# Kernel tuning notes

Hardware: AMD Instinct MI355X
Metric: run time of the kernel (lower is better)

## Reference

```python
import jax, jax.numpy as jnp
import numpy as np

H, C = 3, 64          # heads, out_channels
NEG_SLOPE = 0.2       # PyG GATConv leaky_relu default
LN_EPS = 1e-5


def setup_inputs() -> dict:
    key = jax.random.key(0)
    ks = jax.random.split(key, 20)
    N, E, D_in, edge_dim = 50000, 800000, 64, 5
    g = lambda k, shape: (jax.random.normal(k, shape, dtype=jnp.float32) * 0.1)
    return {
        "x": jax.random.normal(ks[0], (N, D_in), dtype=jnp.float32),
        "edge_attr": jax.random.normal(ks[1], (E, edge_dim), dtype=jnp.float32),
        "lin_w": g(ks[2], (D_in, H * C)),          # GATConv.lin (bias=False)
        "att_src": g(ks[3], (H, C)),
        "att_dst": g(ks[4], (H, C)),
        "lin_edge_w": g(ks[5], (edge_dim, H * C)),  # GATConv.lin_edge (bias=False)
        "att_edge": g(ks[6], (H, C)),
        "gat_bias": jnp.zeros((H * C,), jnp.float32),
        "w1": g(ks[7], (H * C, C)),
        "b1": jnp.zeros((C,), jnp.float32),
        "ln1_g": jnp.ones((C,), jnp.float32),
        "ln1_b": jnp.zeros((C,), jnp.float32),
        "w2": g(ks[8], (C, C)),
        "b2": jnp.zeros((C,), jnp.float32),
        "ln2_g": jnp.ones((C,), jnp.float32),
        "ln2_b": jnp.zeros((C,), jnp.float32),
        "edge_index": jax.random.randint(ks[9], (2, E), 0, N),
    }


def layer_norm(x, g, b):
    m = jnp.mean(x, axis=-1, keepdims=True)
    v = jnp.mean((x - m) ** 2, axis=-1, keepdims=True)
    return (x - m) * jax.lax.rsqrt(v + LN_EPS) * g + b


def gat_conv(x, edge_index, edge_attr, lin_w, att_src, att_dst,
             lin_edge_w, att_edge, gat_bias):
    N = x.shape[0]
    src, dst = edge_index[0], edge_index[1]

    # add_self_loops=True with fill_value='mean': self-loop edge_attr is the
    # per-node mean of incoming edge attributes (0 if node has no in-edges).
    attr_sum = jax.ops.segment_sum(edge_attr, dst, num_segments=N)       # [N, edge_dim]
    cnt = jax.ops.segment_sum(jnp.ones((dst.shape[0],), edge_attr.dtype), dst, num_segments=N)
    loop_attr = attr_sum / jnp.maximum(cnt, 1.0)[:, None]
    loop = jnp.arange(N, dtype=src.dtype)
    src = jnp.concatenate([src, loop])
    dst = jnp.concatenate([dst, loop])
    ea = jnp.concatenate([edge_attr, loop_attr], axis=0)                  # [E2, edge_dim]

    xs = (x @ lin_w).reshape(N, H, C)                                     # [N, H, C]
    a_src = jnp.einsum('nhc,hc->nh', xs, att_src)                         # [N, H]
    a_dst = jnp.einsum('nhc,hc->nh', xs, att_dst)                         # [N, H]
    e = (ea @ lin_edge_w).reshape(-1, H, C)                               # [E2, H, C]
    a_edge = jnp.einsum('ehc,hc->eh', e, att_edge)                        # [E2, H]

    logits = a_src[src] + a_dst[dst] + a_edge                             # [E2, H]
    logits = jnp.where(logits >= 0, logits, NEG_SLOPE * logits)           # leaky_relu

    # segment softmax over incoming edges of each dst node (self loops ensure non-empty)
    lmax = jax.ops.segment_max(logits, dst, num_segments=N)               # [N, H]
    ex = jnp.exp(logits - lmax[dst])
    denom = jax.ops.segment_sum(ex, dst, num_segments=N)                  # [N, H]
    alpha = ex / denom[dst]                                               # [E2, H]

    msgs = alpha[:, :, None] * xs[src]                                    # [E2, H, C]
    out = jax.ops.segment_sum(msgs, dst, num_segments=N)                  # [N, H, C]
    return out.reshape(N, H * C) + gat_bias


def reference(x, edge_attr, lin_w, att_src, att_dst, lin_edge_w, att_edge,
              gat_bias, w1, b1, ln1_g, ln1_b, w2, b2, ln2_g, ln2_b, edge_index):
    x_gat = gat_conv(x, edge_index, edge_attr, lin_w, att_src, att_dst,
                     lin_edge_w, att_edge, gat_bias)
    x_gat = x_gat @ w1 + b1                         # linear1: [N, C]
    x_gat = layer_norm(x + x_gat, ln1_g, ln1_b)     # layerNorm1(x + x_gat)
    lin = x_gat @ w2 + b2                           # linear2
    out = layer_norm(lin + x_gat, ln2_g, ln2_b)     # layerNorm2(lin + x_gat)
    return out                                      # dropout p=0 -> identity
```

## Files before the change

kernel.cpp:

```cpp
#include <hip/hip_runtime.h>


#define HH 3
#define CC 64
#define DIN 64
#define ED 5
#define HC 192
#define NEG_SLOPE 0.2f
#define LN_EPS 1e-5f
#define LOG2E 1.44269504f

typedef __attribute__((ext_vector_type(8))) short bf16x8;
typedef __attribute__((ext_vector_type(4))) float f32x4;

__device__ __forceinline__ float leaky(float l) { return fmaxf(l, NEG_SLOPE * l); }

__device__ __forceinline__ unsigned short f2bf(float f) {
    unsigned u = __float_as_uint(f);
    unsigned r = (u + 0x7FFFu + ((u >> 16) & 1u)) >> 16;
    return (unsigned short)r;
}
__device__ __forceinline__ float bf2f(unsigned short u) {
    return __uint_as_float((unsigned)u << 16);
}
__device__ __forceinline__ float bf_lo(unsigned v) { return __uint_as_float(v << 16); }
__device__ __forceinline__ float bf_hi(unsigned v) { return __uint_as_float(v & 0xFFFF0000u); }

__device__ __forceinline__ bf16x8 pack8(float4 a, float4 b) {
    bf16x8 r;
    r[0] = (short)f2bf(a.x); r[1] = (short)f2bf(a.y);
    r[2] = (short)f2bf(a.z); r[3] = (short)f2bf(a.w);
    r[4] = (short)f2bf(b.x); r[5] = (short)f2bf(b.y);
    r[6] = (short)f2bf(b.z); r[7] = (short)f2bf(b.w);
    return r;
}

#define PREP_TOT (HC*DIN + DIN*HC + CC*CC + CC + ED*HH)
#define PREP_BLOCKS 30
__global__ __launch_bounds__(256) void k_prep_cnt(const float* __restrict__ lin_w,
                                                  const float* __restrict__ w1,
                                                  const float* __restrict__ w2,
                                                  const float* __restrict__ b1,
                                                  const float* __restrict__ gat_bias,
                                                  const float* __restrict__ lin_edge_w,
                                                  const float* __restrict__ att_edge,
                                                  unsigned short* __restrict__ linwt,
                                                  unsigned short* __restrict__ w1t,
                                                  unsigned short* __restrict__ w2t,
                                                  float* __restrict__ b1p,
                                                  float* __restrict__ we,
                                                  const int* __restrict__ ei,
                                                  int* __restrict__ icnt, int E) {
    if (blockIdx.x < PREP_BLOCKS) {
        for (int i = blockIdx.x * 256 + threadIdx.x; i < PREP_TOT; i += PREP_BLOCKS * 256) {
            if (i < HC * DIN) {
                int c = i >> 6, k = i & 63;
                linwt[i] = f2bf(lin_w[k * HC + c]);
            } else if (i < 2 * HC * DIN) {
                int j = i - HC * DIN;
                int c = j / HC, k = j - c * HC;
                w1t[j] = f2bf(w1[k * CC + c]);
            } else if (i < 2 * HC * DIN + CC * CC) {
                int j = i - 2 * HC * DIN;
                int c = j >> 6, k = j & 63;
                w2t[j] = f2bf(w2[k * CC + c]);
            } else if (i < 2 * HC * DIN + CC * CC + CC) {
                int c = i - (2 * HC * DIN + CC * CC);
                float s = b1[c];
                for (int k = 0; k < HC; ++k) s += gat_bias[k] * w1[k * CC + c];
                b1p[c] = s;
            } else {
                int q = i - (2 * HC * DIN + CC * CC + CC);
                int d = q / HH, h = q - d * HH;
                float s = 0.f;
                for (int c = 0; c < CC; ++c)
                    s += lin_edge_w[d * HC + h * CC + c] * att_edge[h * CC + c];
                we[q] = s * LOG2E;
            }
        }
    } else {
        int nb = gridDim.x - PREP_BLOCKS;
        for (int e = (blockIdx.x - PREP_BLOCKS) * 256 + threadIdx.x; e < E; e += nb * 256)
            atomicAdd(&icnt[ei[E + e]], 1);
    }
}

__global__ __launch_bounds__(256) void k_xs(const float* __restrict__ x,
                                            const unsigned short* __restrict__ linwt,
                                            const float* __restrict__ att_src,
                                            const float* __restrict__ att_dst,
                                            unsigned short* __restrict__ xsb,
                                            float* __restrict__ a_src,
                                            float* __restrict__ a_dst, int N) {
    int lane = threadIdx.x & 63, w = threadIdx.x >> 6;
    int l15 = lane & 15, kg = (lane >> 4) * 8;
    int nb = blockIdx.x * 64;
    int arow = nb + w * 16 + l15;
    int arow_c = min(arow, N - 1);

    f32x4 acc[12];
    #pragma unroll
    for (int ct = 0; ct < 12; ++ct) acc[ct] = (f32x4){0.f, 0.f, 0.f, 0.f};

    #pragma unroll
    for (int k0 = 0; k0 < DIN; k0 += 32) {
        const float* ap = x + (size_t)arow_c * DIN + k0 + kg;
        float4 a0 = *(const float4*)ap;
        float4 a1 = *(const float4*)(ap + 4);
        bf16x8 af = pack8(a0, a1);
        #pragma unroll
        for (int ct = 0; ct < 12; ++ct) {
            bf16x8 bf = *(const bf16x8*)(linwt + (size_t)(ct * 16 + l15) * DIN + k0 + kg);
            acc[ct] = __builtin_amdgcn_mfma_f32_16x16x32_bf16(af, bf, acc[ct], 0, 0, 0);
        }
    }

    float asv[12], adv[12];
    #pragma unroll
    for (int ct = 0; ct < 12; ++ct) {
        int c = ct * 16 + l15;
        asv[ct] = att_src[c]; adv[ct] = att_dst[c];
    }

    int rbase = nb + w * 16 + (lane >> 4) * 4;
    #pragma unroll
    for (int j = 0; j < 4; ++j) {
        int r = rbase + j;
        bool ok = r < N;
        float ps0 = 0.f, ps1 = 0.f, ps2 = 0.f, pd0 = 0.f, pd1 = 0.f, pd2 = 0.f;
        #pragma unroll
        for (int ct = 0; ct < 12; ++ct) {
            float v = acc[ct][j];
            float s = v * asv[ct], d = v * adv[ct];
            if (ct < 4)      { ps0 += s; pd0 += d; }
            else if (ct < 8) { ps1 += s; pd1 += d; }
            else             { ps2 += s; pd2 += d; }
        }
        if (ok) {
            unsigned* row32 = (unsigned*)(xsb + (size_t)r * HC);
            #pragma unroll
            for (int ct = 0; ct < 4; ++ct) {
                int c = ct * 16 + l15;
                row32[c] = (unsigned)f2bf(acc[ct][j]) | ((unsigned)f2bf(acc[ct + 4][j]) << 16);
                xsb[(size_t)r * HC + 128 + c] = f2bf(acc[ct + 8][j]);
            }
        }
        #pragma unroll
        for (int o = 1; o < 16; o <<= 1) {
            ps0 += __shfl_xor(ps0, o, 64); pd0 += __shfl_xor(pd0, o, 64);
            ps1 += __shfl_xor(ps1, o, 64); pd1 += __shfl_xor(pd1, o, 64);
            ps2 += __shfl_xor(ps2, o, 64); pd2 += __shfl_xor(pd2, o, 64);
        }
        if (ok && l15 == 0) {
            a_src[r * HH + 0] = ps0 * LOG2E; a_src[r * HH + 1] = ps1 * LOG2E;
            a_src[r * HH + 2] = ps2 * LOG2E;
            a_dst[r * HH + 0] = pd0 * LOG2E; a_dst[r * HH + 1] = pd1 * LOG2E;
            a_dst[r * HH + 2] = pd2 * LOG2E;
        }
    }
}

__global__ __launch_bounds__(256) void k_scan1(const int* __restrict__ icnt,
                                               int* __restrict__ bsum, int N) {
    int i = blockIdx.x * 256 + threadIdx.x;
    int lane = threadIdx.x & 63, wid = threadIdx.x >> 6;
    int v = (i < N) ? icnt[i] : 0;
    #pragma unroll
    for (int o = 32; o; o >>= 1) v += __shfl_xor(v, o, 64);
    __shared__ int wt[4];
    if (lane == 0) wt[wid] = v;
    __syncthreads();
    if (threadIdx.x == 0) bsum[blockIdx.x] = wt[0] + wt[1] + wt[2] + wt[3];
}

__global__ __launch_bounds__(1024) void k_scan2(const int* __restrict__ bsum,
                                                int* __restrict__ boff, int nb) {
    __shared__ int s[1024];
    int t = threadIdx.x;
    int v = (t < nb) ? bsum[t] : 0;
    s[t] = v;
    __syncthreads();
    for (int d = 1; d < 1024; d <<= 1) {
        int u = (t >= d) ? s[t - d] : 0;
        __syncthreads();
        s[t] += u;
        __syncthreads();
    }
    if (t < nb) boff[t] = s[t] - v;
}

__global__ __launch_bounds__(256) void k_scan3(const int* __restrict__ icnt,
                                               const int* __restrict__ boff,
                                               int* __restrict__ off,
                                               int* __restrict__ cursor, int N) {
    int i = blockIdx.x * 256 + threadIdx.x;
    int lane = threadIdx.x & 63, wid = threadIdx.x >> 6;
    int v = (i < N) ? icnt[i] : 0;
    int incl = v;
    #pragma unroll
    for (int o = 1; o < 64; o <<= 1) {
        int u = __shfl_up(incl, o, 64);
        if (lane >= o) incl += u;
    }
    __shared__ int wt[4];
    if (lane == 63) wt[wid] = incl;
    __syncthreads();
    int wpre = 0;
    for (int w = 0; w < wid; ++w) wpre += wt[w];
    int excl = boff[blockIdx.x] + wpre + incl - v;
    if (i < N) {
        off[i] = excl;
        cursor[i] = excl;
        if (i == N - 1) off[N] = excl + v;
    }
}

__global__ __launch_bounds__(256) void k_fill(const float* __restrict__ ea,
                                              const int* __restrict__ ei,
                                              const float* __restrict__ a_src,
                                              const float* __restrict__ a_dst,
                                              const float* __restrict__ we,
                                              int* __restrict__ cursor,
                                              uint4* __restrict__ payload, int E) {
    int e = blockIdx.x * blockDim.x + threadIdx.x;
    if (e >= E) return;
    int s = ei[e], d = ei[E + e];
    float attr[ED];
    #pragma unroll
    for (int j = 0; j < ED; ++j) attr[j] = ea[(size_t)e * ED + j];
    float aeh[HH], lp[HH];
    #pragma unroll
    for (int h = 0; h < HH; ++h) {
        float a = 0.f;
        #pragma unroll
        for (int j = 0; j < ED; ++j) a += attr[j] * we[j * HH + h];
        aeh[h] = a;
        lp[h] = a_src[s * HH + h] + a_dst[d * HH + h] + a;
    }
    int pos = atomicAdd(&cursor[d], 1);
    uint4 pk;
    pk.x = (unsigned)f2bf(lp[0])  | ((unsigned)f2bf(lp[1])  << 16);
    pk.y = (unsigned)f2bf(lp[2])  | ((unsigned)f2bf(aeh[0]) << 16);
    pk.z = (unsigned)f2bf(aeh[1]) | ((unsigned)f2bf(aeh[2]) << 16);
    pk.w = (unsigned)s;
    payload[pos] = pk;
}

__global__ __launch_bounds__(256) void k_gat(const unsigned short* __restrict__ xsb,
                                             const float* __restrict__ a_src,
                                             const float* __restrict__ a_dst,
                                             const int* __restrict__ off,
                                             const uint4* __restrict__ payload,
                                             unsigned short* __restrict__ oaccb, int N) {
    __shared__ float4 wbuf[4][64];
    int lane = threadIdx.x & 63;
    int wid  = threadIdx.x >> 6;
    const unsigned* xs32 = (const unsigned*)xsb;
    unsigned c128ml = 128u - (unsigned)lane;
    for (int n = blockIdx.x * 4 + wid; n < N; n += gridDim.x * 4) {
        int beg = off[n], end = off[n + 1];
        int deg = end - beg;

        float pden0 = 0.f, pden1 = 0.f, pden2 = 0.f;
        float pae0 = 0.f, pae1 = 0.f, pae2 = 0.f;
        float a0A = 0.f, a1A = 0.f, a2A = 0.f;
        float a0B = 0.f, a1B = 0.f, a2B = 0.f;

        for (int c0 = 0; c0 < deg; c0 += 64) {
            int cn = min(deg - c0, 64);
            float w0 = 0.f, w1 = 0.f, w2 = 0.f;
            int src = 0;
            if (lane < cn) {
                uint4 p = payload[beg + c0 + lane];
                w0 = exp2f(leaky(bf_lo(p.x)));
                w1 = exp2f(leaky(bf_hi(p.x)));
                w2 = exp2f(leaky(bf_lo(p.y)));
                pae0 += bf_hi(p.y);
                pae1 += bf_lo(p.z);
                pae2 += bf_hi(p.z);
                pden0 += w0; pden1 += w1; pden2 += w2;
                src = (int)p.w;
            }
            wbuf[wid][lane] = make_float4(w0, w1, w2, __int_as_float(src));
            int i = 0;
            for (; i + 2 <= cn; i += 2) {
                float4 ta = wbuf[wid][i];
                float4 tb = wbuf[wid][i + 1];
                unsigned ia = __umul24((unsigned)__float_as_int(ta.w), 96u) + lane;
                unsigned ib = __umul24((unsigned)__float_as_int(tb.w), 96u) + lane;
                unsigned va = xs32[ia];
                unsigned vb = xs32[ib];
                float xa2 = bf2f(xsb[(ia << 1) + c128ml]);
                float xb2 = bf2f(xsb[(ib << 1) + c128ml]);
                a0A += ta.x * bf_lo(va); a1A += ta.y * bf_hi(va); a2A += ta.z * xa2;
                a0B += tb.x * bf_lo(vb); a1B += tb.y * bf_hi(vb); a2B += tb.z * xb2;
            }
            if (i < cn) {
                float4 ta = wbuf[wid][i];
                unsigned ia = __umul24((unsigned)__float_as_int(ta.w), 96u) + lane;
                unsigned va = xs32[ia];
                a0A += ta.x * bf_lo(va);
                a1A += ta.y * bf_hi(va);
                a2A += ta.z * bf2f(xsb[(ia << 1) + c128ml]);
            }
        }

        #pragma unroll
        for (int o = 32; o; o >>= 1) {
            pden0 += __shfl_xor(pden0, o, 64);
            pden1 += __shfl_xor(pden1, o, 64);
            pden2 += __shfl_xor(pden2, o, 64);
            pae0  += __shfl_xor(pae0, o, 64);
            pae1  += __shfl_xor(pae1, o, 64);
            pae2  += __shfl_xor(pae2, o, 64);
        }

        float dc = fmaxf((float)deg, 1.0f);
        float inv_dc = __builtin_amdgcn_rcpf(dc);
        float sl0 = leaky(a_src[n * HH + 0] + a_dst[n * HH + 0] + pae0 * inv_dc);
        float sl1 = leaky(a_src[n * HH + 1] + a_dst[n * HH + 1] + pae1 * inv_dc);
        float sl2 = leaky(a_src[n * HH + 2] + a_dst[n * HH + 2] + pae2 * inv_dc);
        float e0 = exp2f(sl0), e1 = exp2f(sl1), e2 = exp2f(sl2);
        unsigned ian = __umul24((unsigned)n, 96u) + lane;
        unsigned van = xs32[ian];
        float xn2 = bf2f(xsb[(ian << 1) + c128ml]);
        float r0 = __builtin_amdgcn_rcpf(pden0 + e0);
        float r1 = __builtin_amdgcn_rcpf(pden1 + e1);
        float r2 = __builtin_amdgcn_rcpf(pden2 + e2);
        float acc0 = (a0A + a0B + e0 * bf_lo(van)) * r0;
        float acc1 = (a1A + a1B + e1 * bf_hi(van)) * r1;
        float acc2 = (a2A + a2B + e2 * xn2) * r2;
        size_t nbse = (size_t)n * HC;
        oaccb[nbse + 0 * CC + lane] = f2bf(acc0);
        oaccb[nbse + 1 * CC + lane] = f2bf(acc1);
        oaccb[nbse + 2 * CC + lane] = f2bf(acc2);
    }
}

__global__ __launch_bounds__(256) void k_mlp(const unsigned short* __restrict__ oaccb,
                                             const unsigned short* __restrict__ w1t,
                                             const unsigned short* __restrict__ w2t,
                                             const float* __restrict__ b1p,
                                             const float* __restrict__ x,
                                             const float* __restrict__ g1,
                                             const float* __restrict__ be1,
                                             const float* __restrict__ b2,
                                             const float* __restrict__ g2,
                                             const float* __restrict__ be2,
                                             float* __restrict__ out, int N) {
    __shared__ unsigned short H1[64 * 72];
    int lane = threadIdx.x & 63, w = threadIdx.x >> 6;
    int l15 = lane & 15, kg = (lane >> 4) * 8;
    int nb = blockIdx.x * 64;
    int arow = nb + w * 16 + l15;
    int arow_c = min(arow, N - 1);

    float c_b1[4], c_g1[4], c_be1[4], c_b2[4], c_g2[4], c_be2[4];
    #pragma unroll
    for (int ct = 0; ct < 4; ++ct) {
        int c = ct * 16 + l15;
        c_b1[ct] = b1p[c]; c_g1[ct] = g1[c]; c_be1[ct] = be1[c];
        c_b2[ct] = b2[c];  c_g2[ct] = g2[c]; c_be2[ct] = be2[c];
    }

    f32x4 acc[4];
    #pragma unroll
    for (int ct = 0; ct < 4; ++ct) acc[ct] = (f32x4){0.f, 0.f, 0.f, 0.f};
    #pragma unroll
    for (int k0 = 0; k0 < HC; k0 += 32) {
        bf16x8 af = *(const bf16x8*)(oaccb + (size_t)arow_c * HC + k0 + kg);
        #pragma unroll
        for (int ct = 0; ct < 4; ++ct) {
            bf16x8 bf = *(const bf16x8*)(w1t + (size_t)(ct * 16 + l15) * HC + k0 + kg);
            acc[ct] = __builtin_amdgcn_mfma_f32_16x16x32_bf16(af, bf, acc[ct], 0, 0, 0);
        }
    }

    int rbase = nb + w * 16 + (lane >> 4) * 4;
    int rloc0 = w * 16 + (lane >> 4) * 4;
    float h1v[4][4];
    float y[4][4];
    #pragma unroll
    for (int j = 0; j < 4; ++j) {
        int r = min(rbase + j, N - 1);
        #pragma unroll
        for (int ct = 0; ct < 4; ++ct)
            y[ct][j] = acc[ct][j] + c_b1[ct] + x[(size_t)r * DIN + ct * 16 + l15];
    }
    #pragma unroll
    for (int j = 0; j < 4; ++j) {
        float s = y[0][j] + y[1][j] + y[2][j] + y[3][j];
        #pragma unroll
        for (int o = 1; o < 16; o <<= 1) s += __shfl_xor(s, o, 64);
        float m = s * (1.0f / CC);
        float vs = 0.f;
        #pragma unroll
        for (int ct = 0; ct < 4; ++ct) { float d = y[ct][j] - m; vs += d * d; }
        #pragma unroll
        for (int o = 1; o < 16; o <<= 1) vs += __shfl_xor(vs, o, 64);
        float inv = rsqrtf(vs * (1.0f / CC) + LN_EPS);
        #pragma unroll
        for (int ct = 0; ct < 4; ++ct) {
            float h = (y[ct][j] - m) * inv * c_g1[ct] + c_be1[ct];
            h1v[ct][j] = h;
            H1[(rloc0 + j) * 72 + ct * 16 + l15] = f2bf(h);
        }
    }
    __syncthreads();

    f32x4 acc2[4];
    #pragma unroll
    for (int ct = 0; ct < 4; ++ct) acc2[ct] = (f32x4){0.f, 0.f, 0.f, 0.f};
    #pragma unroll
    for (int k0 = 0; k0 < CC; k0 += 32) {
        bf16x8 af = *(const bf16x8*)&H1[(w * 16 + l15) * 72 + k0 + kg];
        #pragma unroll
        for (int ct = 0; ct < 4; ++ct) {
            bf16x8 bf = *(const bf16x8*)(w2t + (size_t)(ct * 16 + l15) * CC + k0 + kg);
            acc2[ct] = __builtin_amdgcn_mfma_f32_16x16x32_bf16(af, bf, acc2[ct], 0, 0, 0);
        }
    }

    #pragma unroll
    for (int j = 0; j < 4; ++j) {
        float z0 = acc2[0][j] + c_b2[0] + h1v[0][j];
        float z1 = acc2[1][j] + c_b2[1] + h1v[1][j];
        float z2 = acc2[2][j] + c_b2[2] + h1v[2][j];
        float z3 = acc2[3][j] + c_b2[3] + h1v[3][j];
        float s = z0 + z1 + z2 + z3;
        #pragma unroll
        for (int o = 1; o < 16; o <<= 1) s += __shfl_xor(s, o, 64);
        float m = s * (1.0f / CC);
        float d0 = z0 - m, d1 = z1 - m, d2 = z2 - m, d3 = z3 - m;
        float vs = d0 * d0 + d1 * d1 + d2 * d2 + d3 * d3;
        #pragma unroll
        for (int o = 1; o < 16; o <<= 1) vs += __shfl_xor(vs, o, 64);
        float inv = rsqrtf(vs * (1.0f / CC) + LN_EPS);
        int r = rbase + j;
        if (r < N) {
            out[(size_t)r * CC + 0 * 16 + l15] = d0 * inv * c_g2[0] + c_be2[0];
            out[(size_t)r * CC + 1 * 16 + l15] = d1 * inv * c_g2[1] + c_be2[1];
            out[(size_t)r * CC + 2 * 16 + l15] = d2 * inv * c_g2[2] + c_be2[2];
            out[(size_t)r * CC + 3 * 16 + l15] = d3 * inv * c_g2[3] + c_be2[3];
        }
    }
}

extern "C" void kernel_launch(void* const* d_in, const int* in_sizes, int n_in,
                              void* d_out, int out_size, void* d_ws, size_t ws_size,
                              hipStream_t stream) {
    const float* x          = (const float*)d_in[0];
    const float* edge_attr  = (const float*)d_in[1];
    const float* lin_w      = (const float*)d_in[2];
    const float* att_src    = (const float*)d_in[3];
    const float* att_dst    = (const float*)d_in[4];
    const float* lin_edge_w = (const float*)d_in[5];
    const float* att_edge   = (const float*)d_in[6];
    const float* gat_bias   = (const float*)d_in[7];
    const float* w1         = (const float*)d_in[8];
    const float* b1         = (const float*)d_in[9];
    const float* ln1_g      = (const float*)d_in[10];
    const float* ln1_b      = (const float*)d_in[11];
    const float* w2         = (const float*)d_in[12];
    const float* b2         = (const float*)d_in[13];
    const float* ln2_g      = (const float*)d_in[14];
    const float* ln2_b      = (const float*)d_in[15];
    const int*   ei         = (const int*)d_in[16];
    float* out = (float*)d_out;

    const int N = in_sizes[0] / DIN;
    const int E = in_sizes[1] / ED;
    const int nb_scan = (N + 255) / 256;

    char* ws = (char*)d_ws;
    size_t off_b = 0;
    auto alloc = [&](size_t bytes) {
        size_t o = off_b;
        off_b = (off_b + bytes + 255) & ~(size_t)255;
        return o;
    };
    int* icnt = (int*)(ws + alloc((size_t)N * 4));
    size_t zero_bytes = off_b;
    unsigned short* xsb   = (unsigned short*)(ws + alloc((size_t)N * HC * 2));
    unsigned short* oaccb = (unsigned short*)(ws + alloc((size_t)N * HC * 2));
    float*  a_srcb  = (float*)(ws + alloc((size_t)N * HH * 4));
    float*  a_dstb  = (float*)(ws + alloc((size_t)N * HH * 4));
    int*    offb    = (int*)(ws + alloc((size_t)(N + 1) * 4));
    int*    cursor  = (int*)(ws + alloc((size_t)N * 4));
    int*    bsum    = (int*)(ws + alloc((size_t)nb_scan * 4));
    int*    boff    = (int*)(ws + alloc((size_t)nb_scan * 4));
    uint4*  payload = (uint4*)(ws + alloc((size_t)E * 16));
    unsigned short* linwt = (unsigned short*)(ws + alloc((size_t)HC * DIN * 2));
    unsigned short* w1t   = (unsigned short*)(ws + alloc((size_t)DIN * HC * 2));
    unsigned short* w2t   = (unsigned short*)(ws + alloc((size_t)CC * CC * 2));
    float* b1p = (float*)(ws + alloc((size_t)CC * 4));
    float* we  = (float*)(ws + alloc((size_t)ED * HH * 4));
    (void)ws_size; (void)n_in; (void)out_size;

    hipMemsetAsync(d_ws, 0, zero_bytes, stream);

    k_prep_cnt<<<PREP_BLOCKS + (E + 255) / 256, 256, 0, stream>>>(
        lin_w, w1, w2, b1, gat_bias, lin_edge_w, att_edge,
        linwt, w1t, w2t, b1p, we, ei, icnt, E);
    k_xs<<<(N + 63) / 64, 256, 0, stream>>>(x, linwt, att_src, att_dst, xsb, a_srcb, a_dstb, N);
    k_scan1<<<nb_scan, 256, 0, stream>>>(icnt, bsum, N);
    k_scan2<<<1, 1024, 0, stream>>>(bsum, boff, nb_scan);
    k_scan3<<<nb_scan, 256, 0, stream>>>(icnt, boff, offb, cursor, N);
    k_fill<<<(E + 255) / 256, 256, 0, stream>>>(edge_attr, ei, a_srcb, a_dstb, we, cursor,
                                                payload, E);
    k_gat<<<(N + 3) / 4, 256, 0, stream>>>(xsb, a_srcb, a_dstb, offb, payload, oaccb, N);
    k_mlp<<<(N + 63) / 64, 256, 0, stream>>>(oaccb, w1t, w2t, b1p, x,
                                             ln1_g, ln1_b, b2, ln2_g, ln2_b, out, N);
}
```

Baseline: 192.1 us.

## Replace three-pass scan with atomic block-offset allocation; broadcast weights via readlane

The three-kernel exclusive scan for CSR offsets is collapsed into a single kernel in which each block claims its base offset with an atomicAdd on a global counter. Segments are therefore no longer in node order, but each node's range stays contiguous, and the GAT kernel now reads degree from icnt instead of off[n+1]. In the GAT aggregation loop, per-edge weights and source indices are broadcast with readlane instead of going through an LDS buffer. This removes two kernel launches and the LDS round trip, at the cost of a nondeterministic payload layout and more scalar readlane instructions.

```diff
diff --git a/kernel.cpp b/kernel.cpp
--- a/kernel.cpp
+++ b/kernel.cpp
@@ -25,6 +25,9 @@
 }
 __device__ __forceinline__ float bf_lo(unsigned v) { return __uint_as_float(v << 16); }
 __device__ __forceinline__ float bf_hi(unsigned v) { return __uint_as_float(v & 0xFFFF0000u); }
+__device__ __forceinline__ float rdl_f(float v, int i) {
+    return __int_as_float(__builtin_amdgcn_readlane(__float_as_int(v), i));
+}
 
 __device__ __forceinline__ bf16x8 pack8(float4 a, float4 b) {
     bf16x8 r;
@@ -160,37 +163,8 @@
     }
 }
 
-__global__ __launch_bounds__(256) void k_scan1(const int* __restrict__ icnt,
-                                               int* __restrict__ bsum, int N) {
-    int i = blockIdx.x * 256 + threadIdx.x;
-    int lane = threadIdx.x & 63, wid = threadIdx.x >> 6;
-    int v = (i < N) ? icnt[i] : 0;
-    #pragma unroll
-    for (int o = 32; o; o >>= 1) v += __shfl_xor(v, o, 64);
-    __shared__ int wt[4];
-    if (lane == 0) wt[wid] = v;
-    __syncthreads();
-    if (threadIdx.x == 0) bsum[blockIdx.x] = wt[0] + wt[1] + wt[2] + wt[3];
-}
-
-__global__ __launch_bounds__(1024) void k_scan2(const int* __restrict__ bsum,
-                                                int* __restrict__ boff, int nb) {
-    __shared__ int s[1024];
-    int t = threadIdx.x;
-    int v = (t < nb) ? bsum[t] : 0;
-    s[t] = v;
-    __syncthreads();
-    for (int d = 1; d < 1024; d <<= 1) {
-        int u = (t >= d) ? s[t - d] : 0;
-        __syncthreads();
-        s[t] += u;
-        __syncthreads();
-    }
-    if (t < nb) boff[t] = s[t] - v;
-}
-
-__global__ __launch_bounds__(256) void k_scan3(const int* __restrict__ icnt,
-                                               const int* __restrict__ boff,
+__global__ __launch_bounds__(256) void k_scanA(const int* __restrict__ icnt,
+                                               int* __restrict__ gtot,
                                                int* __restrict__ off,
                                                int* __restrict__ cursor, int N) {
     int i = blockIdx.x * 256 + threadIdx.x;
@@ -203,15 +177,18 @@
         if (lane >= o) incl += u;
     }
     __shared__ int wt[4];
+    __shared__ int base_sh;
     if (lane == 63) wt[wid] = incl;
+    __syncthreads();
+    if (threadIdx.x == 0)
+        base_sh = atomicAdd(gtot, wt[0] + wt[1] + wt[2] + wt[3]);
     __syncthreads();
     int wpre = 0;
     for (int w = 0; w < wid; ++w) wpre += wt[w];
-    int excl = boff[blockIdx.x] + wpre + incl - v;
+    int excl = base_sh + wpre + incl - v;
     if (i < N) {
         off[i] = excl;
         cursor[i] = excl;
-        if (i == N - 1) off[N] = excl + v;
     }
 }
 
@@ -250,16 +227,16 @@
                                              const float* __restrict__ a_src,
                                              const float* __restrict__ a_dst,
                                              const int* __restrict__ off,
+                                             const int* __restrict__ icnt,
                                              const uint4* __restrict__ payload,
                                              unsigned short* __restrict__ oaccb, int N) {
-    __shared__ float4 wbuf[4][64];
     int lane = threadIdx.x & 63;
     int wid  = threadIdx.x >> 6;
     const unsigned* xs32 = (const unsigned*)xsb;
     unsigned c128ml = 128u - (unsigned)lane;
     for (int n = blockIdx.x * 4 + wid; n < N; n += gridDim.x * 4) {
-        int beg = off[n], end = off[n + 1];
-        int deg = end - beg;
+        int beg = off[n];
+        int deg = icnt[n];
 
         float pden0 = 0.f, pden1 = 0.f, pden2 = 0.f;
         float pae0 = 0.f, pae1 = 0.f, pae2 = 0.f;
@@ -269,7 +246,7 @@
         for (int c0 = 0; c0 < deg; c0 += 64) {
             int cn = min(deg - c0, 64);
             float w0 = 0.f, w1 = 0.f, w2 = 0.f;
-            int src = 0;
+            int srcv = 0;
             if (lane < cn) {
                 uint4 p = payload[beg + c0 + lane];
                 w0 = exp2f(leaky(bf_lo(p.x)));
@@ -279,29 +256,31 @@
                 pae1 += bf_lo(p.z);
                 pae2 += bf_hi(p.z);
                 pden0 += w0; pden1 += w1; pden2 += w2;
-                src = (int)p.w;
+                srcv = (int)p.w;
             }
-            wbuf[wid][lane] = make_float4(w0, w1, w2, __int_as_float(src));
             int i = 0;
             for (; i + 2 <= cn; i += 2) {
-                float4 ta = wbuf[wid][i];
-                float4 tb = wbuf[wid][i + 1];
-                unsigned ia = __umul24((unsigned)__float_as_int(ta.w), 96u) + lane;
-                unsigned ib = __umul24((unsigned)__float_as_int(tb.w), 96u) + lane;
+                float ta0 = rdl_f(w0, i),     ta1 = rdl_f(w1, i),     ta2 = rdl_f(w2, i);
+                int   sa  = __builtin_amdgcn_readlane(srcv, i);
+                float tb0 = rdl_f(w0, i + 1), tb1 = rdl_f(w1, i + 1), tb2 = rdl_f(w2, i + 1);
+                int   sb  = __builtin_amdgcn_readlane(srcv, i + 1);
+                unsigned ia = (unsigned)sa * 96u + lane;
+                unsigned ib = (unsigned)sb * 96u + lane;
                 unsigned va = xs32[ia];
                 unsigned vb = xs32[ib];
                 float xa2 = bf2f(xsb[(ia << 1) + c128ml]);
                 float xb2 = bf2f(xsb[(ib << 1) + c128ml]);
-                a0A += ta.x * bf_lo(va); a1A += ta.y * bf_hi(va); a2A += ta.z * xa2;
-                a0B += tb.x * bf_lo(vb); a1B += tb.y * bf_hi(vb); a2B += tb.z * xb2;
+                a0A += ta0 * bf_lo(va); a1A += ta1 * bf_hi(va); a2A += ta2 * xa2;
+                a0B += tb0 * bf_lo(vb); a1B += tb1 * bf_hi(vb); a2B += tb2 * xb2;
             }
             if (i < cn) {
-                float4 ta = wbuf[wid][i];
-                unsigned ia = __umul24((unsigned)__float_as_int(ta.w), 96u) + lane;
+                float ta0 = rdl_f(w0, i), ta1 = rdl_f(w1, i), ta2 = rdl_f(w2, i);
+                int   sa  = __builtin_amdgcn_readlane(srcv, i);
+                unsigned ia = (unsigned)sa * 96u + lane;
                 unsigned va = xs32[ia];
-                a0A += ta.x * bf_lo(va);
-                a1A += ta.y * bf_hi(va);
-                a2A += ta.z * bf2f(xsb[(ia << 1) + c128ml]);
+                a0A += ta0 * bf_lo(va);
+                a1A += ta1 * bf_hi(va);
+                a2A += ta2 * bf2f(xsb[(ia << 1) + c128ml]);
             }
         }
 
@@ -321,7 +300,7 @@
         float sl1 = leaky(a_src[n * HH + 1] + a_dst[n * HH + 1] + pae1 * inv_dc);
         float sl2 = leaky(a_src[n * HH + 2] + a_dst[n * HH + 2] + pae2 * inv_dc);
         float e0 = exp2f(sl0), e1 = exp2f(sl1), e2 = exp2f(sl2);
-        unsigned ian = __umul24((unsigned)n, 96u) + lane;
+        unsigned ian = (unsigned)n * 96u + lane;
         unsigned van = xs32[ian];
         float xn2 = bf2f(xsb[(ian << 1) + c128ml]);
         float r0 = __builtin_amdgcn_rcpf(pden0 + e0);
@@ -480,15 +459,14 @@
         return o;
     };
     int* icnt = (int*)(ws + alloc((size_t)N * 4));
+    int* gtot = (int*)(ws + alloc(4));
     size_t zero_bytes = off_b;
     unsigned short* xsb   = (unsigned short*)(ws + alloc((size_t)N * HC * 2));
     unsigned short* oaccb = (unsigned short*)(ws + alloc((size_t)N * HC * 2));
     float*  a_srcb  = (float*)(ws + alloc((size_t)N * HH * 4));
     float*  a_dstb  = (float*)(ws + alloc((size_t)N * HH * 4));
-    int*    offb    = (int*)(ws + alloc((size_t)(N + 1) * 4));
+    int*    offb    = (int*)(ws + alloc((size_t)N * 4));
     int*    cursor  = (int*)(ws + alloc((size_t)N * 4));
-    int*    bsum    = (int*)(ws + alloc((size_t)nb_scan * 4));
-    int*    boff    = (int*)(ws + alloc((size_t)nb_scan * 4));
     uint4*  payload = (uint4*)(ws + alloc((size_t)E * 16));
     unsigned short* linwt = (unsigned short*)(ws + alloc((size_t)HC * DIN * 2));
     unsigned short* w1t   = (unsigned short*)(ws + alloc((size_t)DIN * HC * 2));
@@ -503,12 +481,10 @@
         lin_w, w1, w2, b1, gat_bias, lin_edge_w, att_edge,
         linwt, w1t, w2t, b1p, we, ei, icnt, E);
     k_xs<<<(N + 63) / 64, 256, 0, stream>>>(x, linwt, att_src, att_dst, xsb, a_srcb, a_dstb, N);
-    k_scan1<<<nb_scan, 256, 0, stream>>>(icnt, bsum, N);
-    k_scan2<<<1, 1024, 0, stream>>>(bsum, boff, nb_scan);
-    k_scan3<<<nb_scan, 256, 0, stream>>>(icnt, boff, offb, cursor, N);
+    k_scanA<<<nb_scan, 256, 0, stream>>>(icnt, gtot, offb, cursor, N);
     k_fill<<<(E + 255) / 256, 256, 0, stream>>>(edge_attr, ei, a_srcb, a_dstb, we, cursor,
                                                 payload, E);
-    k_gat<<<(N + 3) / 4, 256, 0, stream>>>(xsb, a_srcb, a_dstb, offb, payload, oaccb, N);
+    k_gat<<<(N + 3) / 4, 256, 0, stream>>>(xsb, a_srcb, a_dstb, offb, icnt, payload, oaccb, N);
     k_mlp<<<(N + 63) / 64, 256, 0, stream>>>(oaccb, w1t, w2t, b1p, x,
                                              ln1_g, ln1_b, b2, ln2_g, ln2_b, out, N);
 }
```

Measured after the change: 186.9 us. 1.03x faster.
